# Optimization experiments

Hardware: AMD Instinct MI355X
Metric: run time of the kernel (lower is better)

## Reference

```python
import jax, jax.numpy as jnp
import numpy as np
from jax import lax

B, N, C, H = 16, 577, 1024, 16
D = C // H          # head_dim = 64
M = 24              # spatial side, M*M = N-1
CH = C // 4         # conv bottleneck channels = 256
EPS = 1e-5


def _ln(x, g, b):
    mu = jnp.mean(x, axis=-1, keepdims=True)
    var = jnp.mean((x - mu) ** 2, axis=-1, keepdims=True)
    return (x - mu) * lax.rsqrt(var + EPS) * g + b


def setup_inputs() -> dict:
    key = jax.random.key(0)
    ks = jax.random.split(key, 8)
    s = 0.02
    return {
        "x": jax.random.normal(ks[0], (B, N, C), jnp.float32),
        "ln1_g": jnp.ones((C,), jnp.float32),
        "ln1_b": jnp.zeros((C,), jnp.float32),
        "in_w": jax.random.normal(ks[1], (3 * C, C), jnp.float32) * s,
        "in_b": jnp.zeros((3 * C,), jnp.float32),
        "out_w": jax.random.normal(ks[2], (C, C), jnp.float32) * s,
        "out_b": jnp.zeros((C,), jnp.float32),
        "ln2_g": jnp.ones((C,), jnp.float32),
        "ln2_b": jnp.zeros((C,), jnp.float32),
        "conv1_w": jax.random.normal(ks[3], (CH, C, 3, 3), jnp.float32) * s,
        "conv1_b": jnp.zeros((CH,), jnp.float32),
        "conv2_w": jax.random.normal(ks[4], (C, CH, 3, 3), jnp.float32) * s,
        "conv2_b": jnp.zeros((C,), jnp.float32),
    }


def reference(x, ln1_g, ln1_b, in_w, in_b, out_w, out_b, ln2_g, ln2_b,
              conv1_w, conv1_b, conv2_w, conv2_b):
    residual = x
    h = _ln(x, ln1_g, ln1_b)
    # qkv projection: (B,N,3C) -> (3,B,H,N,D)
    qkv = (h @ in_w.T + in_b).reshape(B, N, 3, H, D).transpose(2, 0, 3, 1, 4)
    q, k, v = qkv[0], qkv[1], qkv[2]
    scale = D ** (-0.5)
    scores = jnp.einsum("bhnd,bhmd->bhnm", q, k) * scale   # (B,H,N,N)
    attn = jax.nn.softmax(scores, axis=-1)
    o = jnp.einsum("bhnm,bhmd->bhnd", attn, v)
    o = o.transpose(0, 2, 1, 3).reshape(B, N, C)
    o = o @ out_w.T + out_b
    x = o + residual                                       # first residual

    y = _ln(x, ln2_g, ln2_b)
    f = y[:, :-1, :].reshape(B, M, M, C).transpose(0, 3, 1, 2)   # NCHW
    c = y[:, -1:, :]                                             # class token
    f = lax.conv_general_dilated(f, conv1_w, (1, 1), "SAME",
                                 dimension_numbers=("NCHW", "OIHW", "NCHW"))
    f = jax.nn.gelu(f + conv1_b[None, :, None, None])
    f = lax.conv_general_dilated(f, conv2_w, (1, 1), "SAME",
                                 dimension_numbers=("NCHW", "OIHW", "NCHW"))
    f = f + conv2_b[None, :, None, None]
    f = f.transpose(0, 2, 3, 1).reshape(B, N - 1, C)
    y = jnp.concatenate((f, c), axis=1)
    return x + y
```

## Files before the change

kernel.cpp:

```cpp
#include <hip/hip_runtime.h>

typedef unsigned short u16;
typedef unsigned int u32;
typedef __bf16 bf16x8 __attribute__((ext_vector_type(8)));
typedef float f32x4 __attribute__((ext_vector_type(4)));

#define DEVI __device__ __forceinline__

#define BB 16
#define NN 577
#define CC 1024
#define HH 16
#define DD 64
#define BN 9232
#define PIX 576
#define WW 24
#define CHN 256
#define VROW 584
#define PSZ (9216 * 256)

DEVI u16 f2b(float f) {
  u32 u = __builtin_bit_cast(u32, f);
  u32 r = 0x7FFFu + ((u >> 16) & 1u);
  return (u16)((u + r) >> 16);
}

DEVI float b2f(u16 h) { return __builtin_bit_cast(float, (u32)h << 16); }

DEVI bf16x8 ldfrag(const u16* p) {
  uint4 u = *(const uint4*)p;
  return __builtin_bit_cast(bf16x8, u);
}

DEVI f32x4 mfma16(bf16x8 a, bf16x8 b, f32x4 c) {
  return __builtin_amdgcn_mfma_f32_16x16x32_bf16(a, b, c, 0, 0, 0);
}

DEVI void gld_lds16(const u16* g, u16* l) {
  __builtin_amdgcn_global_load_lds((const __attribute__((address_space(1))) void*)g,
                                   (__attribute__((address_space(3))) void*)l, 16, 0, 0);
}

DEVI float gelu_tanh(float v) {
  const float x3 = v * v * v;
  const float t = __expf(1.5957691216057308f * (v + 0.044715f * x3));
  const float th = (t - 1.f) / (t + 1.f);
  return 0.5f * v * (1.f + th);
}

__global__ __launch_bounds__(256) void prep_kernel(
    const float* __restrict__ in_w, const float* __restrict__ out_w,
    const float* __restrict__ c1w, const float* __restrict__ c2w,
    u16* __restrict__ wqkv, u16* __restrict__ wout,
    u16* __restrict__ w1t, u16* __restrict__ w2t, u16* __restrict__ zpad) {
  const int i0 = blockIdx.x * 256 + threadIdx.x;
  const int stride = gridDim.x * 256;
  for (int i = i0; i < 3072 * 1024; i += stride) wqkv[i] = f2b(in_w[i]);
  for (int i = i0; i < 1024 * 1024; i += stride) wout[i] = f2b(out_w[i]);
  for (int i = i0; i < 256 * 9216; i += stride) {
    int oc = i / 9216, rem = i - oc * 9216, tap = rem >> 10, c = rem & 1023;
    w1t[i] = f2b(c1w[(size_t)oc * 9216 + c * 9 + tap]);
  }
  for (int i = i0; i < 1024 * 2304; i += stride) {
    int oc = i / 2304, rem = i - oc * 2304, tap = rem >> 8, c = rem & 255;
    w2t[i] = f2b(c2w[(size_t)oc * 2304 + c * 9 + tap]);
  }
  if (i0 < 128) zpad[i0] = 0;
}

template <int MODE>
__global__ __launch_bounds__(256) void ln_kernel(
    const float* __restrict__ xf, const u16* __restrict__ xh,
    const float* __restrict__ gam, const float* __restrict__ bet,
    u16* __restrict__ yout, float* __restrict__ oextra) {
  __shared__ float sh[8];
  const int row = blockIdx.x;
  const int tid = threadIdx.x;
  float4 v;
  if constexpr (MODE == 0) {
    v = ((const float4*)(xf + (size_t)row * CC))[tid];
  } else {
    ushort4 uv = ((const ushort4*)(xh + (size_t)row * CC))[tid];
    v = make_float4(b2f(uv.x), b2f(uv.y), b2f(uv.z), b2f(uv.w));
  }
  float s = v.x + v.y + v.z + v.w;
  float qq = v.x * v.x + v.y * v.y + v.z * v.z + v.w * v.w;
#pragma unroll
  for (int off = 32; off > 0; off >>= 1) {
    s += __shfl_down(s, off);
    qq += __shfl_down(qq, off);
  }
  if ((tid & 63) == 0) { sh[tid >> 6] = s; sh[4 + (tid >> 6)] = qq; }
  __syncthreads();
  s = sh[0] + sh[1] + sh[2] + sh[3];
  qq = sh[4] + sh[5] + sh[6] + sh[7];
  const float mu = s * (1.f / 1024.f);
  const float rstd = rsqrtf(qq * (1.f / 1024.f) - mu * mu + 1e-5f);
  const float4 g4 = ((const float4*)gam)[tid];
  const float4 b4 = ((const float4*)bet)[tid];
  const float o0 = (v.x - mu) * rstd * g4.x + b4.x;
  const float o1 = (v.y - mu) * rstd * g4.y + b4.y;
  const float o2 = (v.z - mu) * rstd * g4.z + b4.z;
  const float o3 = (v.w - mu) * rstd * g4.w + b4.w;
  ushort4 st = make_ushort4(f2b(o0), f2b(o1), f2b(o2), f2b(o3));
  *(ushort4*)(yout + (size_t)row * CC + tid * 4) = st;
  if constexpr (MODE == 1) {
    if (row % NN == NN - 1) {
      float4 ov = make_float4(v.x + o0, v.y + o1, v.z + o2, v.w + o3);
      ((float4*)(oextra + (size_t)row * CC))[tid] = ov;
    }
  }
}

struct GArgs {
  const u16* A; const u16* Bm; const float* bias; const float* res; const u16* resH;
  float* outF; u16* outH; u16* outQ; u16* outK; u16* outV; const u16* zpad;
  int M, K;
};

template <int MODE>
__global__ __launch_bounds__(512, 1) void gemm8_kernel(GArgs ag) {
  __shared__ u16 SH[65536];
  const int tid = threadIdx.x;
  const int w = tid >> 6, l = tid & 63;
  const int wm = w >> 2, wn = w & 3;
  const int lr = l & 15, lg = l >> 4;
  const int orig = blockIdx.x;
  const int xcd = orig & 7;
  int mt, nt = 0, tapz = 0, piece = 0, NST;
  if constexpr (MODE == 0) {
    const int wg = (xcd < 4 ? xcd * 56 : 224 + (xcd - 4) * 55) + (orig >> 3);
    nt = wg / 37; mt = wg - nt * 37;
    NST = 16;
  } else if constexpr (MODE == 2) {
    const int wg = (xcd < 4 ? xcd * 41 : 164 + (xcd - 4) * 40) + (orig >> 3);
    tapz = wg / 36; mt = wg - tapz * 36;
    NST = 16;
  } else {
    const int wg = xcd * 36 + (orig >> 3);
    piece = wg / 144;
    const int rem = wg - piece * 144;
    mt = rem >> 2; nt = rem & 3;
    NST = piece ? 16 : 20;
  }
  const int m0 = mt * 256, n0 = nt * ((MODE == 2) ? 0 : 256);

  const int srow = tid >> 3;
  const int schk = tid & 7;

  auto aSrc = [&](int row, int kt) -> const u16* {
    const int ch = schk ^ (row & 7);
    if constexpr (MODE == 0) {
      int m = m0 + row;
      m = m < ag.M ? m : ag.M - 1;
      return ag.A + (size_t)m * 1024 + kt * 64 + ch * 8;
    } else {
      const int m = m0 + row;
      const int b = m / PIX, p = m - b * PIX;
      const int py = p / WW, px = p - py * WW;
      int tap, c0;
      if constexpr (MODE == 2) { tap = tapz; c0 = kt * 64; }
      else { tap = (piece ? 5 : 0) + (kt >> 2); c0 = (kt & 3) * 64; }
      const int py2 = py + (tap / 3) - 1, px2 = px + (tap % 3) - 1;
      if ((u32)py2 < (u32)WW && (u32)px2 < (u32)WW) {
        if constexpr (MODE == 2)
          return ag.A + ((size_t)(b * NN + py2 * WW + px2) * CC + c0 + ch * 8);
        else
          return ag.A + ((size_t)(b * PIX + py2 * WW + px2) * CHN + c0 + ch * 8);
      }
      return ag.zpad + ch * 8;
    }
  };
  auto bSrc = [&](int row, int kt) -> const u16* {
    const int ch = schk ^ (row & 7);
    if constexpr (MODE == 0)
      return ag.Bm + (size_t)(n0 + row) * 1024 + kt * 64 + ch * 8;
    else if constexpr (MODE == 2)
      return ag.Bm + (size_t)row * 9216 + tapz * 1024 + kt * 64 + ch * 8;
    else
      return ag.Bm + (size_t)(n0 + row) * 2304 + (piece ? 1280 : 0) + kt * 64 + ch * 8;
  };

  auto stageA = [&](int buf, int kt, int j) {
    gld_lds16(aSrc(j * 64 + srow, kt), &SH[buf * 16384 + (j * 64 + w * 8) * 64]);
  };
  auto stageB = [&](int buf, int kt, int j) {
    gld_lds16(bSrc(j * 64 + srow, kt), &SH[32768 + buf * 16384 + (j * 64 + w * 8) * 64]);
  };

  f32x4 acc[8][4] = {};

#pragma unroll
  for (int j = 0; j < 4; ++j) { stageA(0, 0, j); stageB(0, 0, j); }

  for (int kt = 0; kt < NST; ++kt) {
    asm volatile("s_waitcnt vmcnt(0)" ::: "memory");
    __builtin_amdgcn_s_barrier();
    const int bf = kt & 1, nb = bf ^ 1;
    const u16* AB = &SH[bf * 16384];
    const u16* BBm = &SH[32768 + bf * 16384];
    bf16x8 bfr[4];
#pragma unroll
    for (int ph = 0; ph < 4; ++ph) {
      const int mg = (ph & 1) << 2;
      const int kh = ph >> 1;
      bf16x8 af[4];
#pragma unroll
      for (int i = 0; i < 4; ++i) {
        const int ra = wm * 128 + (mg + i) * 16 + lr;
        af[i] = ldfrag(&AB[ra * 64 + (((kh << 2) + lg) ^ (ra & 7)) * 8]);
      }
      if ((ph & 1) == 0) {
#pragma unroll
        for (int i = 0; i < 4; ++i) {
          const int rb = wn * 64 + i * 16 + lr;
          bfr[i] = ldfrag(&BBm[rb * 64 + (((kh << 2) + lg) ^ (rb & 7)) * 8]);
        }
      }
      if (ph == 0 && kt + 1 < NST) {
#pragma unroll
        for (int j = 0; j < 4; ++j) { stageA(nb, kt + 1, j); stageB(nb, kt + 1, j); }
      }
      __builtin_amdgcn_s_barrier();
      asm volatile("s_waitcnt lgkmcnt(0)" ::: "memory");
      __builtin_amdgcn_s_setprio(1);
#pragma unroll
      for (int mi = 0; mi < 4; ++mi)
#pragma unroll
        for (int ni = 0; ni < 4; ++ni)
          acc[mg + mi][ni] = mfma16(af[mi], bfr[ni], acc[mg + mi][ni]);
      __builtin_amdgcn_s_setprio(0);
      __builtin_amdgcn_s_barrier();
    }
  }

  if constexpr (MODE == 2) {
    const int tl = (tapz < 5) ? tapz : tapz - 5;
    u16* pb = (tapz < 5) ? ag.outH : ag.outQ;
#pragma unroll
    for (int mi = 0; mi < 8; ++mi) {
#pragma unroll
      for (int r = 0; r < 4; ++r) {
        const int row = m0 + wm * 128 + mi * 16 + (lg << 2) + r;
#pragma unroll
        for (int ni = 0; ni < 4; ++ni) {
          const int col = wn * 64 + ni * 16 + lr;
          pb[(size_t)tl * PSZ + (size_t)row * CHN + col] = f2b(acc[mi][ni][r]);
        }
      }
    }
    return;
  } else if constexpr (MODE == 3) {
    u16* pb = piece ? ag.outQ : ag.outH;
#pragma unroll
    for (int mi = 0; mi < 8; ++mi) {
#pragma unroll
      for (int r = 0; r < 4; ++r) {
        const int row = m0 + wm * 128 + mi * 16 + (lg << 2) + r;
#pragma unroll
        for (int ni = 0; ni < 4; ++ni) {
          const int col = n0 + wn * 64 + ni * 16 + lr;
          pb[(size_t)row * CC + col] = f2b(acc[mi][ni][r]);
        }
      }
    }
    return;
  } else {
    if (n0 >= 2048) {
      __syncthreads();
      const int hh = (n0 + wn * 64 - 2048) >> 6;
      u16* scr = SH + w * 5120;
#pragma unroll
      for (int qh = 0; qh < 2; ++qh) {
        if (qh) { asm volatile("s_waitcnt lgkmcnt(0)" ::: "memory"); }
        const int G0 = m0 + wm * 128 + qh * 64;
        const int b0q = G0 / NN;
        const bool ok = (G0 + 63 < ag.M) && (b0q == (G0 + 63) / NN);
        if (ok) {
#pragma unroll
          for (int mi = 0; mi < 4; ++mi) {
#pragma unroll
            for (int ni = 0; ni < 4; ++ni) {
              const f32x4 a4 = acc[qh * 4 + mi][ni];
              const float bv = ag.bias[n0 + wn * 64 + ni * 16 + lr];
              ushort4 st;
              st.x = f2b(a4[0] + bv);
              st.y = f2b(a4[1] + bv);
              st.z = f2b(a4[2] + bv);
              st.w = f2b(a4[3] + bv);
              *(ushort4*)(scr + (ni * 16 + lr) * 80 + mi * 16 + lg * 4) = st;
            }
          }
          asm volatile("s_waitcnt lgkmcnt(0)" ::: "memory");
          const int nb2 = G0 - b0q * NN;
          u16* vb = ag.outV + (size_t)((b0q * 16 + hh) * 64) * VROW;
#pragma unroll
          for (int pass = 0; pass < 8; ++pass) {
            const int d_ = pass * 8 + (l >> 3);
            const int nn = (l & 7) * 8;
            uint4 vv = *(const uint4*)(scr + d_ * 80 + nn);
            u16* dst = vb + (size_t)d_ * VROW + nb2 + nn;
            if (!(nb2 & 1)) {
              ((u32*)dst)[0] = vv.x; ((u32*)dst)[1] = vv.y;
              ((u32*)dst)[2] = vv.z; ((u32*)dst)[3] = vv.w;
            } else {
              u16 tmp[8];
              *(uint4*)tmp = vv;
#pragma unroll
              for (int j = 0; j < 8; ++j) dst[j] = tmp[j];
            }
          }
        } else {
#pragma unroll
          for (int mi = 0; mi < 4; ++mi) {
#pragma unroll
            for (int r = 0; r < 4; ++r) {
              const int row = G0 + mi * 16 + lg * 4 + r;
              if (row >= ag.M) continue;
              const int b = row / NN, n = row - b * NN;
#pragma unroll
              for (int ni = 0; ni < 4; ++ni) {
                const int col = n0 + wn * 64 + ni * 16 + lr;
                const int d = col & 63;
                const float v = acc[qh * 4 + mi][ni][r] + ag.bias[col];
                ag.outV[((size_t)((b * 16 + hh) * 64 + d)) * VROW + n] = f2b(v);
              }
            }
          }
        }
      }
      return;
    }
    const bool isQ = n0 < 1024;
#pragma unroll
    for (int mi = 0; mi < 8; ++mi) {
#pragma unroll
      for (int r = 0; r < 4; ++r) {
        const int row = m0 + wm * 128 + mi * 16 + (lg << 2) + r;
        if (row >= ag.M) continue;
        const int b = row / NN, n = row - b * NN;
#pragma unroll
        for (int ni = 0; ni < 4; ++ni) {
          const int col = n0 + wn * 64 + ni * 16 + lr;
          const int hd = col & 1023, h = hd >> 6, d = hd & 63;
          const float v = acc[mi][ni][r] + ag.bias[col];
          if (isQ)
            ag.outQ[((size_t)(b * 16 + h) * NN + n) * DD + d] = f2b(v * 0.18033688011112042f);
          else
            ag.outK[((size_t)(b * 16 + h) * NN + n) * DD + d] = f2b(v);
        }
      }
    }
  }
}

template <int MODE>
__global__ __launch_bounds__(256) void gemm_kernel(GArgs ag) {
  __shared__ u16 SH[24576];
  const int tid = threadIdx.x;
  const int w = tid >> 6, l = tid & 63;
  const int wr = w >> 1, wc = w & 1;
  const int lr = l & 15, lg = l >> 4;
  const int bid = blockIdx.x;
  const int nt = bid & 7, mt = bid >> 3;
  const int m0 = mt * 128, n0 = nt * 128;
  const int rA = w * 16 + (l >> 2);
  const int cbs = ((l & 3) ^ ((l >> 3) & 3)) * 8;

  auto stage = [&](int buf, int kt) {
    const int k0 = kt * 32;
    u16* Ald = SH + buf * 4096;
    u16* Bld = SH + 12288 + buf * 4096;
#pragma unroll
    for (int c = 0; c < 2; ++c) {
      const int r = c * 64 + rA;
      int m = m0 + r;
      m = m < ag.M ? m : ag.M - 1;
      gld_lds16(ag.A + (size_t)m * ag.K + (k0 + cbs), &Ald[c * 2048 + w * 512]);
      gld_lds16(ag.Bm + (size_t)(n0 + r) * ag.K + (k0 + cbs), &Bld[c * 2048 + w * 512]);
    }
  };

  f32x4 acc[4][4] = {};
  const int nst = ag.K >> 5;

  stage(0, 0);
  stage(1, 1);

  const int swz = (lr >> 1) & 3;
  int b0 = 0, b1 = 1, b2 = 2;
  for (int kt = 0; kt < nst; ++kt) {
    if (kt + 1 < nst) { asm volatile("s_waitcnt vmcnt(4)" ::: "memory"); }
    else              { asm volatile("s_waitcnt vmcnt(0)" ::: "memory"); }
    __builtin_amdgcn_s_barrier();
    if (kt + 2 < nst) stage(b2, kt + 2);
    bf16x8 af[4], bfr[4];
#pragma unroll
    for (int i = 0; i < 4; ++i)
      af[i] = ldfrag(&SH[b0 * 4096 + (wr * 64 + i * 16 + lr) * 32 + ((lg ^ swz) * 8)]);
#pragma unroll
    for (int i = 0; i < 4; ++i)
      bfr[i] = ldfrag(&SH[12288 + b0 * 4096 + (wc * 64 + i * 16 + lr) * 32 + ((lg ^ swz) * 8)]);
    __builtin_amdgcn_s_setprio(1);
#pragma unroll
    for (int mi = 0; mi < 4; ++mi)
#pragma unroll
      for (int ni = 0; ni < 4; ++ni) acc[mi][ni] = mfma16(af[mi], bfr[ni], acc[mi][ni]);
    __builtin_amdgcn_s_setprio(0);
    const int tmp = b0; b0 = b1; b1 = b2; b2 = tmp;
  }

#pragma unroll
  for (int mi = 0; mi < 4; ++mi) {
#pragma unroll
    for (int r = 0; r < 4; ++r) {
      const int row = m0 + wr * 64 + mi * 16 + lg * 4 + r;
      if (row >= ag.M) continue;
#pragma unroll
      for (int ni = 0; ni < 4; ++ni) {
        const int col = n0 + wc * 64 + ni * 16 + lr;
        const size_t idx = (size_t)row * CC + col;
        ag.outH[idx] = f2b(acc[mi][ni][r] + ag.bias[col] + ag.res[idx]);
      }
    }
  }
}

__global__ __launch_bounds__(256) void gelu_reduce_kernel(
    const u16* __restrict__ pA, const u16* __restrict__ pB,
    const float* __restrict__ bias, u16* __restrict__ f1) {
  const size_t i4 = ((size_t)blockIdx.x * 256 + threadIdx.x) * 4;
  const int col = (int)(i4 & 255);
  float s0 = 0.f, s1 = 0.f, s2 = 0.f, s3 = 0.f;
#pragma unroll
  for (int t = 0; t < 5; ++t) {
    ushort4 u = *(const ushort4*)(pA + (size_t)t * PSZ + i4);
    s0 += b2f(u.x); s1 += b2f(u.y); s2 += b2f(u.z); s3 += b2f(u.w);
  }
#pragma unroll
  for (int t = 0; t < 4; ++t) {
    ushort4 u = *(const ushort4*)(pB + (size_t)t * PSZ + i4);
    s0 += b2f(u.x); s1 += b2f(u.y); s2 += b2f(u.z); s3 += b2f(u.w);
  }
  const float4 b4 = *(const float4*)(bias + col);
  ushort4 st = make_ushort4(f2b(gelu_tanh(s0 + b4.x)), f2b(gelu_tanh(s1 + b4.y)),
                            f2b(gelu_tanh(s2 + b4.z)), f2b(gelu_tanh(s3 + b4.w)));
  *(ushort4*)(f1 + i4) = st;
}

__global__ __launch_bounds__(256) void conv2_combine_kernel(
    const u16* __restrict__ p0, const u16* __restrict__ p1,
    const float* __restrict__ bias, const u16* __restrict__ x2h,
    float* __restrict__ out) {
  const size_t i4 = ((size_t)blockIdx.x * 256 + threadIdx.x) * 4;
  const int col = (int)(i4 & 1023);
  const int row = (int)(i4 >> 10);
  const int b = row / PIX, p = row - b * PIX;
  const ushort4 a = *(const ushort4*)(p0 + i4);
  const ushort4 c = *(const ushort4*)(p1 + i4);
  const size_t oidx = ((size_t)(b * NN + p) << 10) + col;
  const ushort4 xh = *(const ushort4*)(x2h + oidx);
  const float4 bv = *(const float4*)(bias + col);
  float4 o;
  o.x = b2f(a.x) + b2f(c.x) + bv.x + b2f(xh.x);
  o.y = b2f(a.y) + b2f(c.y) + bv.y + b2f(xh.y);
  o.z = b2f(a.z) + b2f(c.z) + bv.z + b2f(xh.z);
  o.w = b2f(a.w) + b2f(c.w) + bv.w + b2f(xh.w);
  *(float4*)(out + oidx) = o;
}

__global__ __launch_bounds__(512) void attn_kernel(
    const u16* __restrict__ q, const u16* __restrict__ k,
    const u16* __restrict__ vt, u16* __restrict__ o) {
  __shared__ u16 SH2[24576];
  const int tid = threadIdx.x;
  const int w = tid >> 6, l = tid & 63;
  const int lr = l & 15, lg = l >> 4;
  const int lg4 = lg * 4;
  const int bid = blockIdx.x;
  const int xcd = bid & 7, gg = bid >> 3;
  const int bh = (gg / 5) * 8 + xcd;
  const int qt = gg % 5;
  const int b = bh >> 4, h = bh & 15;

  const u16* qp = q + (size_t)bh * NN * DD;
  const u16* kp = k + (size_t)bh * NN * DD;
  const u16* vp = vt + (size_t)bh * DD * VROW;

  const int qrow = qt * 128 + w * 16 + lr;
  const int qrc = qrow < NN ? qrow : NN - 1;
  const bf16x8 qf0 = ldfrag(qp + (size_t)qrc * DD + lg * 8);
  const bf16x8 qf1 = ldfrag(qp + (size_t)qrc * DD + 32 + lg * 8);

  const int srow = l >> 3;
  const int schk = (l & 7) ^ (srow & 7);
  auto stage = [&](int buf, int kt) {
    const int kb = kt * 64;
    gld_lds16(kp + (size_t)(kb + w * 8 + srow) * DD + schk * 8,
              &SH2[buf * 4096 + w * 512]);
    gld_lds16(vp + (size_t)(w * 8 + srow) * VROW + kb + schk * 8,
              &SH2[8192 + buf * 4096 + w * 512]);
  };

  f32x4 oa[4] = {};
  float mrow = -1e30f;
  float lsum = 0.f;
  u16* pw = &SH2[16384 + w * 1024];
  const int x7 = lr & 7;
  const int x3 = lr & 3;

  stage(0, 0);
  stage(1, 1);

  for (int kt = 0; kt < 10; ++kt) {
    if (kt <= 7) { asm volatile("s_waitcnt vmcnt(2)" ::: "memory"); }
    else         { asm volatile("s_waitcnt vmcnt(0)" ::: "memory"); }
    __builtin_amdgcn_s_barrier();
    const u16* KB = &SH2[(kt & 1) * 4096];
    const u16* VB = &SH2[8192 + (kt & 1) * 4096];
    const int kb = kt * 64;

    f32x4 s[4] = {};
#pragma unroll
    for (int g = 0; g < 4; ++g) {
      const int row = g * 16 + lr;
      const bf16x8 a0 = ldfrag(&KB[row * 64 + ((lg ^ x7) * 8)]);
      const bf16x8 a1 = ldfrag(&KB[row * 64 + (((4 + lg) ^ x7) * 8)]);
      s[g] = mfma16(a0, qf0, s[g]);
      s[g] = mfma16(a1, qf1, s[g]);
    }
    float t[16];
    const bool last = (kt == 9);
#pragma unroll
    for (int g = 0; g < 4; ++g)
#pragma unroll
      for (int r = 0; r < 4; ++r) {
        const int key = kb + g * 16 + lg4 + r;
        t[g * 4 + r] = (!last || key < NN) ? s[g][r] : -3e38f;
      }
    float pmax = t[0];
#pragma unroll
    for (int i = 1; i < 16; ++i) pmax = fmaxf(pmax, t[i]);
    pmax = fmaxf(pmax, __shfl_xor(pmax, 16));
    pmax = fmaxf(pmax, __shfl_xor(pmax, 32));
    if (!__all(pmax <= mrow + 8.f)) {
      const float mn = fmaxf(mrow, pmax);
      const float corr = exp2f(mrow - mn);
      mrow = mn;
      lsum *= corr;
      float bc[4];
#pragma unroll
      for (int r = 0; r < 4; ++r) bc[r] = __shfl(corr, (l & 48) | (lg4 + r));
#pragma unroll
      for (int g = 0; g < 4; ++g)
#pragma unroll
        for (int r = 0; r < 4; ++r) oa[g][r] *= bc[r];
    }
    float ps[16];
    float rsum = 0.f;
#pragma unroll
    for (int i = 0; i < 16; ++i) { ps[i] = exp2f(t[i] - mrow); rsum += ps[i]; }
    rsum += __shfl_xor(rsum, 16);
    rsum += __shfl_xor(rsum, 32);
    lsum += rsum;
#pragma unroll
    for (int g = 0; g < 4; ++g) {
      u32 w0, w1;
      asm("v_cvt_pk_bf16_f32 %0, %1, %2" : "=v"(w0) : "v"(ps[g * 4 + 0]), "v"(ps[g * 4 + 1]));
      asm("v_cvt_pk_bf16_f32 %0, %1, %2" : "=v"(w1) : "v"(ps[g * 4 + 2]), "v"(ps[g * 4 + 3]));
      const int lc = (g & 1) * 2 + (lg >> 1);
      const int off = (g >> 1) * 512 + lr * 32 + ((lc ^ x3) * 8) + (lg & 1) * 4;
      *(uint2*)(&pw[off]) = make_uint2(w0, w1);
    }
    asm volatile("s_waitcnt lgkmcnt(0)" ::: "memory");
    const bf16x8 paf = ldfrag(&pw[lr * 32 + ((lg ^ x3) * 8)]);
    const bf16x8 pbf = ldfrag(&pw[512 + lr * 32 + ((lg ^ x3) * 8)]);
#pragma unroll
    for (int dg = 0; dg < 4; ++dg) {
      const int row = dg * 16 + lr;
      const bf16x8 v0 = ldfrag(&VB[row * 64 + ((lg ^ x7) * 8)]);
      const bf16x8 v1 = ldfrag(&VB[row * 64 + (((4 + lg) ^ x7) * 8)]);
      oa[dg] = mfma16(paf, v0, oa[dg]);
      oa[dg] = mfma16(pbf, v1, oa[dg]);
    }
    asm volatile("s_waitcnt lgkmcnt(0)" ::: "memory");
    __builtin_amdgcn_s_barrier();
    if (kt + 2 <= 9) stage(kt & 1, kt + 2);
  }

  const int nq = qt * 128 + w * 16 + lg4;
  float linv[4];
#pragma unroll
  for (int r = 0; r < 4; ++r) linv[r] = __shfl(lsum, (l & 48) | (lg4 + r));
#pragma unroll
  for (int r = 0; r < 4; ++r) {
    const int n = nq + r;
    if (n >= NN) continue;
    const float inv = 1.0f / linv[r];
#pragma unroll
    for (int g = 0; g < 4; ++g)
      o[(size_t)(b * NN + n) * CC + h * DD + g * 16 + lr] = f2b(oa[g][r] * inv);
  }
}

extern "C" void kernel_launch(void* const* d_in, const int* in_sizes, int n_in,
                              void* d_out, int out_size, void* d_ws, size_t ws_size,
                              hipStream_t stream) {
  const float* x     = (const float*)d_in[0];
  const float* ln1_g = (const float*)d_in[1];
  const float* ln1_b = (const float*)d_in[2];
  const float* in_w  = (const float*)d_in[3];
  const float* in_b  = (const float*)d_in[4];
  const float* out_w = (const float*)d_in[5];
  const float* out_b = (const float*)d_in[6];
  const float* ln2_g = (const float*)d_in[7];
  const float* ln2_b = (const float*)d_in[8];
  const float* c1w   = (const float*)d_in[9];
  const float* c1b   = (const float*)d_in[10];
  const float* c2w   = (const float*)d_in[11];
  const float* c2b   = (const float*)d_in[12];
  float* out = (float*)d_out;

  char* ws = (char*)d_ws;
  size_t off = 0;
  auto alloc = [&](size_t bytes) {
    void* p = ws + off;
    off += (bytes + 255) & ~(size_t)255;
    return p;
  };
  u16* hb   = (u16*)alloc((size_t)BN * CC * 2);
  u16* wqkv = (u16*)alloc((size_t)3072 * 1024 * 2);
  u16* wout = (u16*)alloc((size_t)1024 * 1024 * 2);
  u16* w1t  = (u16*)alloc((size_t)256 * 9216 * 2);
  u16* w2t  = (u16*)alloc((size_t)1024 * 2304 * 2);
  u16* qb   = (u16*)alloc((size_t)256 * NN * DD * 2);
  u16* kb   = (u16*)alloc((size_t)256 * NN * DD * 2);
  u16* vtb  = (u16*)alloc((size_t)256 * DD * VROW * 2 + 16384);
  u16* x2h  = (u16*)alloc((size_t)BN * CC * 2);
  u16* zpad = (u16*)alloc(256);
  u16* ob = hb;
  u16* yb = qb;
  u16* f1 = kb;
  u16* pA = hb;
  u16* pB = vtb;

  prep_kernel<<<1024, 256, 0, stream>>>(in_w, out_w, c1w, c2w, wqkv, wout, w1t, w2t, zpad);
  ln_kernel<0><<<BN, 256, 0, stream>>>(x, nullptr, ln1_g, ln1_b, hb, nullptr);
  {
    GArgs a{hb, wqkv, in_b, nullptr, nullptr, nullptr, nullptr, qb, kb, vtb, zpad, BN, CC};
    gemm8_kernel<0><<<444, 512, 0, stream>>>(a);
  }
  attn_kernel<<<1280, 512, 0, stream>>>(qb, kb, vtb, ob);
  {
    GArgs a{ob, wout, out_b, x, nullptr, nullptr, x2h, nullptr, nullptr, nullptr, zpad, BN, CC};
    gemm_kernel<1><<<584, 256, 0, stream>>>(a);
  }
  ln_kernel<1><<<BN, 256, 0, stream>>>(nullptr, x2h, ln2_g, ln2_b, yb, out);
  {
    GArgs a{yb, w1t, c1b, nullptr, nullptr, nullptr, pA, pB, nullptr, nullptr, zpad, 9216, 9216};
    gemm8_kernel<2><<<324, 512, 0, stream>>>(a);
  }
  gelu_reduce_kernel<<<2304, 256, 0, stream>>>(pA, pB, c1b, f1);
  {
    GArgs a{f1, w2t, c2b, nullptr, nullptr, nullptr, hb, vtb, nullptr, nullptr, zpad, 9216, 2304};
    gemm8_kernel<3><<<288, 512, 0, stream>>>(a);
  }
  conv2_combine_kernel<<<9216, 256, 0, stream>>>(hb, vtb, c2b, x2h, out);
}
```

Before: 408.0 us.

## Split GEMM K-tile staging into two halves with partial vmcnt waits

Changes the LDS layout of each 64-wide K tile into two 32-wide halves, each with its own XOR swizzle, and stages the next tile one half at a time. Each half waits only with vmcnt(4) before its barrier, so compute on the first half can begin while loads for the second half are still in flight. This finer-grained pipelining aims to cut load stall time in the main GEMM loop. The cost is an extra barrier per tile and a new swizzle pattern that may add LDS bank conflicts.

```diff
diff --git a/kernel.cpp b/kernel.cpp
--- a/kernel.cpp
+++ b/kernel.cpp
@@ -145,81 +145,91 @@
   }
   const int m0 = mt * 256, n0 = nt * ((MODE == 2) ? 0 : 256);
 
-  const int srow = tid >> 3;
-  const int schk = tid & 7;
-
-  auto aSrc = [&](int row, int kt) -> const u16* {
-    const int ch = schk ^ (row & 7);
+  const int srow4 = tid >> 2;
+  const int schk4 = tid & 3;
+
+  auto aSrcH = [&](int row, int kt, int kh) -> const u16* {
+    const int ch = schk4 ^ ((row >> 1) & 3);
+    const int kc = kt * 64 + kh * 32 + ch * 8;
     if constexpr (MODE == 0) {
       int m = m0 + row;
       m = m < ag.M ? m : ag.M - 1;
-      return ag.A + (size_t)m * 1024 + kt * 64 + ch * 8;
+      return ag.A + (size_t)m * 1024 + kc;
     } else {
       const int m = m0 + row;
       const int b = m / PIX, p = m - b * PIX;
       const int py = p / WW, px = p - py * WW;
       int tap, c0;
-      if constexpr (MODE == 2) { tap = tapz; c0 = kt * 64; }
-      else { tap = (piece ? 5 : 0) + (kt >> 2); c0 = (kt & 3) * 64; }
+      if constexpr (MODE == 2) { tap = tapz; c0 = kc; }
+      else { tap = (piece ? 5 : 0) + (kt >> 2); c0 = (kt & 3) * 64 + kh * 32 + ch * 8; }
       const int py2 = py + (tap / 3) - 1, px2 = px + (tap % 3) - 1;
       if ((u32)py2 < (u32)WW && (u32)px2 < (u32)WW) {
         if constexpr (MODE == 2)
-          return ag.A + ((size_t)(b * NN + py2 * WW + px2) * CC + c0 + ch * 8);
+          return ag.A + ((size_t)(b * NN + py2 * WW + px2) * CC + c0);
         else
-          return ag.A + ((size_t)(b * PIX + py2 * WW + px2) * CHN + c0 + ch * 8);
+          return ag.A + ((size_t)(b * PIX + py2 * WW + px2) * CHN + c0);
       }
       return ag.zpad + ch * 8;
     }
   };
-  auto bSrc = [&](int row, int kt) -> const u16* {
-    const int ch = schk ^ (row & 7);
+  auto bSrcH = [&](int row, int kt, int kh) -> const u16* {
+    const int ch = schk4 ^ ((row >> 1) & 3);
+    const int kc = kt * 64 + kh * 32 + ch * 8;
     if constexpr (MODE == 0)
-      return ag.Bm + (size_t)(n0 + row) * 1024 + kt * 64 + ch * 8;
+      return ag.Bm + (size_t)(n0 + row) * 1024 + kc;
     else if constexpr (MODE == 2)
-      return ag.Bm + (size_t)row * 9216 + tapz * 1024 + kt * 64 + ch * 8;
+      return ag.Bm + (size_t)row * 9216 + tapz * 1024 + kc;
     else
-      return ag.Bm + (size_t)(n0 + row) * 2304 + (piece ? 1280 : 0) + kt * 64 + ch * 8;
+      return ag.Bm + (size_t)(n0 + row) * 2304 + (piece ? 1280 : 0) + kc;
   };
 
-  auto stageA = [&](int buf, int kt, int j) {
-    gld_lds16(aSrc(j * 64 + srow, kt), &SH[buf * 16384 + (j * 64 + w * 8) * 64]);
+  auto stageHalf = [&](int buf, int kt, int kh) {
+#pragma unroll
+    for (int j = 0; j < 2; ++j)
+      gld_lds16(aSrcH(j * 128 + srow4, kt, kh),
+                &SH[buf * 16384 + kh * 8192 + j * 4096 + w * 512]);
+#pragma unroll
+    for (int j = 0; j < 2; ++j)
+      gld_lds16(bSrcH(j * 128 + srow4, kt, kh),
+                &SH[32768 + buf * 16384 + kh * 8192 + j * 4096 + w * 512]);
   };
-  auto stageB = [&](int buf, int kt, int j) {
-    gld_lds16(bSrc(j * 64 + srow, kt), &SH[32768 + buf * 16384 + (j * 64 + w * 8) * 64]);
-  };
 
   f32x4 acc[8][4] = {};
 
-#pragma unroll
-  for (int j = 0; j < 4; ++j) { stageA(0, 0, j); stageB(0, 0, j); }
+  stageHalf(0, 0, 0);
+  stageHalf(0, 0, 1);
 
   for (int kt = 0; kt < NST; ++kt) {
-    asm volatile("s_waitcnt vmcnt(0)" ::: "memory");
-    __builtin_amdgcn_s_barrier();
     const int bf = kt & 1, nb = bf ^ 1;
-    const u16* AB = &SH[bf * 16384];
-    const u16* BBm = &SH[32768 + bf * 16384];
     bf16x8 bfr[4];
 #pragma unroll
-    for (int ph = 0; ph < 4; ++ph) {
-      const int mg = (ph & 1) << 2;
-      const int kh = ph >> 1;
+    for (int p = 0; p < 4; ++p) {
+      const int kh = p >> 1;
+      const int mg = (p & 1) << 2;
+      if (p == 0) {
+        asm volatile("s_waitcnt vmcnt(4)" ::: "memory");
+        __builtin_amdgcn_s_barrier();
+        if (kt + 1 < NST) stageHalf(nb, kt + 1, 0);
+      } else if (p == 2) {
+        if (kt + 1 < NST) { asm volatile("s_waitcnt vmcnt(4)" ::: "memory"); }
+        else              { asm volatile("s_waitcnt vmcnt(0)" ::: "memory"); }
+        __builtin_amdgcn_s_barrier();
+        if (kt + 1 < NST) stageHalf(nb, kt + 1, 1);
+      }
+      const u16* AB = &SH[bf * 16384 + kh * 8192];
+      const u16* BBm = &SH[32768 + bf * 16384 + kh * 8192];
       bf16x8 af[4];
 #pragma unroll
       for (int i = 0; i < 4; ++i) {
         const int ra = wm * 128 + (mg + i) * 16 + lr;
-        af[i] = ldfrag(&AB[ra * 64 + (((kh << 2) + lg) ^ (ra & 7)) * 8]);
-      }
-      if ((ph & 1) == 0) {
+        af[i] = ldfrag(&AB[ra * 32 + ((lg ^ ((ra >> 1) & 3)) * 8)]);
+      }
+      if ((p & 1) == 0) {
 #pragma unroll
         for (int i = 0; i < 4; ++i) {
           const int rb = wn * 64 + i * 16 + lr;
-          bfr[i] = ldfrag(&BBm[rb * 64 + (((kh << 2) + lg) ^ (rb & 7)) * 8]);
+          bfr[i] = ldfrag(&BBm[rb * 32 + ((lg ^ ((rb >> 1) & 3)) * 8)]);
         }
-      }
-      if (ph == 0 && kt + 1 < NST) {
-#pragma unroll
-        for (int j = 0; j < 4; ++j) { stageA(nb, kt + 1, j); stageB(nb, kt + 1, j); }
       }
       __builtin_amdgcn_s_barrier();
       asm volatile("s_waitcnt lgkmcnt(0)" ::: "memory");
```

Result: slower. 459.3 us (+12.6%).
